# Performance work log

Hardware: AMD Instinct MI355X
Metric: run time of the kernel (lower is better)

The kernel has to match this reference:

```python
import jax, jax.numpy as jnp
import numpy as np

N_NODES = 50000
N_EDGES = 800000


def _gcn_conv(x, src, dst, norm, W, b, num_nodes):
    # x: [N, Fin] -> h: [N, Fout]; messages gathered from src, scattered to dst.
    h = x @ W
    msgs = h[src] * norm[:, None]                      # [E+N, Fout]
    out = jax.ops.segment_sum(msgs, dst, num_segments=num_nodes)
    return out + b


def _gcn_norm(edge_index, num_nodes):
    # Add self-loops and compute symmetric normalization D^-1/2 (A+I) D^-1/2.
    loops = jnp.arange(num_nodes, dtype=edge_index.dtype)
    src = jnp.concatenate([edge_index[0], loops])
    dst = jnp.concatenate([edge_index[1], loops])
    ones = jnp.ones(src.shape[0], dtype=jnp.float32)
    deg = jax.ops.segment_sum(ones, dst, num_segments=num_nodes)
    dinv = jnp.where(deg > 0, jax.lax.rsqrt(jnp.maximum(deg, 1.0)), 0.0)
    norm = dinv[src] * dinv[dst]
    return src, dst, norm


def setup_inputs() -> dict:
    key = jax.random.key(0)
    k1, k2, k3, k4 = jax.random.split(key, 4)
    map_x = jax.random.normal(k1, (N_NODES, 128), dtype=jnp.float32)
    edge_index = jax.random.randint(k2, (2, N_EDGES), 0, N_NODES, dtype=jnp.int64)
    W1 = jax.random.normal(k3, (128, 64), dtype=jnp.float32) * (1.0 / np.sqrt(128))
    b1 = jnp.zeros((64,), dtype=jnp.float32)
    W2 = jax.random.normal(k4, (64, 32), dtype=jnp.float32) * (1.0 / np.sqrt(64))
    b2 = jnp.zeros((32,), dtype=jnp.float32)
    return {"map": map_x, "edge_index": edge_index, "W1": W1, "b1": b1, "W2": W2, "b2": b2}


def reference(map, edge_index, W1, b1, W2, b2):
    num_nodes = map.shape[0]
    src, dst, norm = _gcn_norm(edge_index, num_nodes)
    x = jax.nn.relu(_gcn_conv(map, src, dst, norm, W1, b1, num_nodes))
    x = jax.nn.relu(_gcn_conv(x, src, dst, norm, W2, b2, num_nodes))
    return x
```

## Files before the change

### kernel.cpp

```cpp
#include <hip/hip_runtime.h>

#define TPB 256
#define ACHUNK 4096
#define BSHIFT 6
#define BNODES 64
#define CAP 2048
#define GROWS 128

__device__ __forceinline__ float blo(unsigned u) { return __uint_as_float(u << 16); }
__device__ __forceinline__ float bhi(unsigned u) { return __uint_as_float(u & 0xffff0000u); }
__device__ __forceinline__ unsigned pack2(float a, float b) {
    unsigned ua = __float_as_uint(a); ua += 0x7fffu + ((ua >> 16) & 1u);
    unsigned ub = __float_as_uint(b); ub += 0x7fffu + ((ub >> 16) & 1u);
    return (ua >> 16) | (ub & 0xffff0000u);
}
__device__ __forceinline__ void dec8(uint4 v, float* f) {
    f[0] = blo(v.x); f[1] = bhi(v.x); f[2] = blo(v.y); f[3] = bhi(v.y);
    f[4] = blo(v.z); f[5] = bhi(v.z); f[6] = blo(v.w); f[7] = bhi(v.w);
}
__device__ __forceinline__ void dec4(uint2 v, float* f) {
    f[0] = blo(v.x); f[1] = bhi(v.x); f[2] = blo(v.y); f[3] = bhi(v.y);
}


__global__ __launch_bounds__(TPB) void k_fat(
        const int* __restrict__ src, const int* __restrict__ dst, int E,
        int* __restrict__ bcnt, int* __restrict__ tmp, int NB,
        const float* __restrict__ X, const float* __restrict__ W,
        unsigned int* __restrict__ H1b, int N, int G1, int FB) {
    __shared__ float Ws[128 * 64];
    int* lcnt = (int*)Ws;
    int bid = blockIdx.x;
    int t = threadIdx.x;

    if ((bid % 3) == 0) {
        int fidx = bid / 3;
        if (fidx >= FB) return;
        int c0 = fidx * ACHUNK;
        int s_[16], d_[16];
#pragma unroll
        for (int i = 0; i < 16; i++) {
            int e = c0 + i * TPB + t;
            if (e < E) { s_[i] = src[e]; d_[i] = dst[e]; }
            else d_[i] = -1;
        }
        for (int b = t; b < NB; b += TPB) lcnt[b] = 0;
        __syncthreads();
#pragma unroll
        for (int i = 0; i < 16; i++)
            if (d_[i] >= 0) atomicAdd(&lcnt[d_[i] >> BSHIFT], 1);
        __syncthreads();
        for (int b = t; b < NB; b += TPB) {
            int c = lcnt[b];
            lcnt[b] = c ? (b * CAP + atomicAdd(&bcnt[b], c)) : 0;
        }
        __syncthreads();
#pragma unroll
        for (int i = 0; i < 16; i++) {
            if (d_[i] >= 0) {
                int bkt = d_[i] >> BSHIFT;
                int pos = atomicAdd(&lcnt[bkt], 1);
                if (pos < (bkt + 1) * CAP) {
                    tmp[pos] = ((d_[i] & (BNODES - 1)) << 16) | s_[i];
                }
            }
        }
    } else {
        int gb = bid - bid / 3 - 1;
        if (gb >= G1) return;
        int row0 = gb * GROWS;

        const float4* W4 = (const float4*)W;
        float4* Ws4 = (float4*)Ws;
#pragma unroll
        for (int i = 0; i < 8; i++) Ws4[t + i * 256] = W4[t + i * 256];
        __syncthreads();

        int rg = t >> 3;
        int c0 = (t & 7) * 8;
        int r0 = row0 + rg * 4;
        int ri[4];
#pragma unroll
        for (int i = 0; i < 4; i++) ri[i] = (r0 + i < N) ? (r0 + i) : (N - 1);

        float acc[4][8];
#pragma unroll
        for (int i = 0; i < 4; i++)
#pragma unroll
            for (int j = 0; j < 8; j++) acc[i][j] = 0.0f;

        const float4* X4 = (const float4*)X;
        for (int kk = 0; kk < 32; kk++) {
            float4 xv[4];
#pragma unroll
            for (int i = 0; i < 4; i++) xv[i] = X4[(size_t)ri[i] * 32 + kk];
#pragma unroll
            for (int q = 0; q < 4; q++) {
                const float* w = Ws + (4 * kk + q) * 64 + c0;
                float wq[8];
#pragma unroll
                for (int j = 0; j < 8; j++) wq[j] = w[j];
                float xq[4];
                xq[0] = q == 0 ? xv[0].x : q == 1 ? xv[0].y : q == 2 ? xv[0].z : xv[0].w;
                xq[1] = q == 0 ? xv[1].x : q == 1 ? xv[1].y : q == 2 ? xv[1].z : xv[1].w;
                xq[2] = q == 0 ? xv[2].x : q == 1 ? xv[2].y : q == 2 ? xv[2].z : xv[2].w;
                xq[3] = q == 0 ? xv[3].x : q == 1 ? xv[3].y : q == 2 ? xv[3].z : xv[3].w;
#pragma unroll
                for (int i = 0; i < 4; i++)
#pragma unroll
                    for (int j = 0; j < 8; j++)
                        acc[i][j] = fmaf(xq[i], wq[j], acc[i][j]);
            }
        }
#pragma unroll
        for (int i = 0; i < 4; i++) {
            if (r0 + i < N) {
                uint4 p = { pack2(acc[i][0], acc[i][1]), pack2(acc[i][2], acc[i][3]),
                            pack2(acc[i][4], acc[i][5]), pack2(acc[i][6], acc[i][7]) };
                *(uint4*)(H1b + (size_t)(r0 + i) * 32 + (t & 7) * 4) = p;
            }
        }
    }
}


__global__ __launch_bounds__(TPB) void k_binB(
        const int* __restrict__ bcnt, const int* __restrict__ tmp,
        int* __restrict__ rowptr, unsigned short* __restrict__ rowlen,
        float* __restrict__ dinv, unsigned short* __restrict__ edges,
        const unsigned int* __restrict__ H1b, unsigned int* __restrict__ g1b,
        int N) {
    __shared__ int hist[BNODES];
    __shared__ int cur[BNODES];
    __shared__ int sh[BNODES];
    __shared__ float dl[BNODES];
    int b = blockIdx.x;
    int t = threadIdx.x;
    int node0 = b << BSHIFT;
    int nn = N - node0; if (nn > BNODES) nn = BNODES;
    int cnt = bcnt[b]; if (cnt > CAP) cnt = CAP;
    const int tb = b * CAP;

    if (t < BNODES) hist[t] = 0;
    __syncthreads();
    for (int i = t; i < cnt; i += TPB) atomicAdd(&hist[tmp[tb + i] >> 16], 1);
    __syncthreads();
    if (t < BNODES) sh[t] = hist[t];
    __syncthreads();
    for (int o = 1; o < BNODES; o <<= 1) {
        int x = (t >= o && t < BNODES) ? sh[t - o] : 0;
        __syncthreads();
        if (t < BNODES) sh[t] += x;
        __syncthreads();
    }
    if (t < BNODES) {
        int v = hist[t];
        int excl = sh[t] - v;
        cur[t] = excl;
        float dv = rsqrtf((float)(v + 1));
        dl[t] = dv;
        if (t < nn) {
            dinv[node0 + t] = dv;
            rowptr[node0 + t] = tb + excl;
            rowlen[node0 + t] = (unsigned short)v;
        }
    }
    __syncthreads();
    for (int i = t; i < cnt; i += TPB) {
        int p = tmp[tb + i];
        int pos = atomicAdd(&cur[p >> 16], 1);
        edges[tb + pos] = (unsigned short)(p & 0xffff);
    }
    const uint4* H4 = (const uint4*)H1b;
    uint4* G4 = (uint4*)g1b;
    for (int i = t; i < nn * 8; i += TPB) {
        int r = i >> 3, q = i & 7;
        float dv = dl[r];
        float f[8];
        uint4 hv = H4[(size_t)(node0 + r) * 8 + q];
        dec8(hv, f);
        uint4 p = { pack2(f[0] * dv, f[1] * dv), pack2(f[2] * dv, f[3] * dv),
                    pack2(f[4] * dv, f[5] * dv), pack2(f[6] * dv, f[7] * dv) };
        G4[(size_t)(node0 + r) * 8 + q] = p;
    }
}


__global__ __launch_bounds__(TPB) void k_gg(
        const int* __restrict__ rowptr, const unsigned short* __restrict__ rowlen,
        const unsigned short* __restrict__ edges,
        const unsigned int* __restrict__ g1b,
        const float* __restrict__ dinv, const float* __restrict__ b1,
        const float* __restrict__ W2, unsigned int* __restrict__ g2b, int N) {
    __shared__ float W2s[64 * 32];
    __shared__ float rows[32 * 68];
    __shared__ float dl[32];
    __shared__ int nst[32];
    __shared__ int nlen[32];
    int t = threadIdx.x;
    int node0 = blockIdx.x * 32;
    int nn = N - node0; if (nn > 32) nn = 32;
    if (nn <= 0) return;

    {
        const float4* W4 = (const float4*)W2;
        float4* Wd = (float4*)W2s;
        Wd[t] = W4[t]; Wd[t + 256] = W4[t + 256];
    }
    if (t < nn) {
        dl[t] = dinv[node0 + t];
        nst[t] = rowptr[node0 + t];
        nlen[t] = rowlen[node0 + t];
    }
    __syncthreads();

    const uint4* G4 = (const uint4*)g1b;
    int nl = t >> 3;
    int lane = t & 7;
    if (nl < nn) {
        float acc[8], f[8];
        uint4 sv = G4[(size_t)(node0 + nl) * 8 + lane];
        dec8(sv, acc);
        int base = nst[nl], deg = nlen[nl];
        int j = 0;
        for (; j + 7 < deg; j += 8) {
            uint4 r[8];
#pragma unroll
            for (int u = 0; u < 8; u++)
                r[u] = G4[(size_t)edges[base + j + u] * 8 + lane];
#pragma unroll
            for (int u = 0; u < 8; u++) {
                dec8(r[u], f);
#pragma unroll
                for (int k = 0; k < 8; k++) acc[k] += f[k];
            }
        }
        for (; j < deg; j++) {
            uint4 r0 = G4[(size_t)edges[base + j] * 8 + lane];
            dec8(r0, f);
#pragma unroll
            for (int k = 0; k < 8; k++) acc[k] += f[k];
        }
        float w0 = dl[nl];
        const float4* bb4 = (const float4*)(b1 + lane * 8);
        float4 ba = bb4[0], bc = bb4[1];
        float* rr = rows + nl * 68 + lane * 8;
        rr[0] = fmaxf(fmaf(acc[0], w0, ba.x), 0.0f);
        rr[1] = fmaxf(fmaf(acc[1], w0, ba.y), 0.0f);
        rr[2] = fmaxf(fmaf(acc[2], w0, ba.z), 0.0f);
        rr[3] = fmaxf(fmaf(acc[3], w0, ba.w), 0.0f);
        rr[4] = fmaxf(fmaf(acc[4], w0, bc.x), 0.0f);
        rr[5] = fmaxf(fmaf(acc[5], w0, bc.y), 0.0f);
        rr[6] = fmaxf(fmaf(acc[6], w0, bc.z), 0.0f);
        rr[7] = fmaxf(fmaf(acc[7], w0, bc.w), 0.0f);
    }
    __syncthreads();

    int n = t >> 3;
    int c = t & 7;
    if (n < nn) {
        const float* row = rows + n * 68;
        float a0 = 0.0f, a1 = 0.0f, a2 = 0.0f, a3 = 0.0f;
#pragma unroll 8
        for (int k = 0; k < 64; k++) {
            float rv = row[k];
            const float* w = W2s + k * 32 + 4 * c;
            a0 = fmaf(rv, w[0], a0); a1 = fmaf(rv, w[1], a1);
            a2 = fmaf(rv, w[2], a2); a3 = fmaf(rv, w[3], a3);
        }
        float dv = dl[n];
        uint2 p = { pack2(a0 * dv, a1 * dv), pack2(a2 * dv, a3 * dv) };
        ((uint2*)g2b)[(size_t)(node0 + n) * 8 + c] = p;
    }
}


__global__ __launch_bounds__(TPB) void k_g32(
        const int* __restrict__ rowptr, const unsigned short* __restrict__ rowlen,
        const unsigned short* __restrict__ edges,
        const unsigned int* __restrict__ g2b,
        const float* __restrict__ dinv, const float* __restrict__ b2,
        float* __restrict__ out, int N) {
    __shared__ float dl[32];
    __shared__ int nst[32];
    __shared__ int nlen[32];
    int t = threadIdx.x;
    int node0 = blockIdx.x * 32;
    int nn = N - node0; if (nn > 32) nn = 32;
    if (nn <= 0) return;
    if (t < nn) {
        dl[t] = dinv[node0 + t];
        nst[t] = rowptr[node0 + t];
        nlen[t] = rowlen[node0 + t];
    }
    __syncthreads();

    int nl = t >> 3;
    int lane = t & 7;
    if (nl >= nn) return;

    const uint2* G2 = (const uint2*)g2b;
    float acc[4], f[4];
    uint2 sv = G2[(size_t)(node0 + nl) * 8 + lane];
    dec4(sv, acc);
    int base = nst[nl], deg = nlen[nl];
    int j = 0;
    for (; j + 15 < deg; j += 16) {
        uint2 r[16];
#pragma unroll
        for (int u = 0; u < 16; u++)
            r[u] = G2[(size_t)edges[base + j + u] * 8 + lane];
#pragma unroll
        for (int u = 0; u < 16; u++) {
            dec4(r[u], f);
            acc[0] += f[0]; acc[1] += f[1]; acc[2] += f[2]; acc[3] += f[3];
        }
    }
    for (; j < deg; j++) {
        uint2 r0 = G2[(size_t)edges[base + j] * 8 + lane];
        dec4(r0, f);
        acc[0] += f[0]; acc[1] += f[1]; acc[2] += f[2]; acc[3] += f[3];
    }
    float w0 = dl[nl];
    const float4* bb4 = (const float4*)(b2 + lane * 4);
    float4 ba = bb4[0];
    float4 o0 = { fmaxf(fmaf(acc[0], w0, ba.x), 0.0f),
                  fmaxf(fmaf(acc[1], w0, ba.y), 0.0f),
                  fmaxf(fmaf(acc[2], w0, ba.z), 0.0f),
                  fmaxf(fmaf(acc[3], w0, ba.w), 0.0f) };
    *(float4*)(out + (size_t)(node0 + nl) * 32 + lane * 4) = o0;
}

static inline int cdiv(int a, int b) { return (a + b - 1) / b; }
static inline char* alignup(char* p) { return (char*)(((uintptr_t)p + 255) & ~(uintptr_t)255); }

extern "C" void kernel_launch(void* const* d_in, const int* in_sizes, int n_in,
                              void* d_out, int out_size, void* d_ws, size_t ws_size,
                              hipStream_t stream) {
    const float* x  = (const float*)d_in[0];
    const int*   ei = (const int*)d_in[1];
    const float* W1 = (const float*)d_in[2];
    const float* b1 = (const float*)d_in[3];
    const float* W2 = (const float*)d_in[4];
    const float* b2 = (const float*)d_in[5];
    float* out = (float*)d_out;

    int N = in_sizes[0] / 128;
    int E = in_sizes[1] / 2;
    const int* src = ei;
    const int* dst = ei + E;

    int NB = cdiv(N, BNODES);

    char* p = (char*)d_ws;
    float* dinv  = (float*)p;            p = alignup(p + sizeof(float) * N);
    int* rowptr  = (int*)p;              p = alignup(p + sizeof(int) * N);
    unsigned short* rowlen = (unsigned short*)p;  p = alignup(p + sizeof(short) * N);
    int* bcnt    = (int*)p;              p = alignup(p + sizeof(int) * 1024);
    int* tmp     = (int*)p;              p = alignup(p + sizeof(int) * (size_t)NB * CAP);
    unsigned short* edges = (unsigned short*)p;   p = alignup(p + sizeof(short) * (size_t)NB * CAP);
    unsigned int* h1b = (unsigned int*)p; p = alignup(p + sizeof(short) * (size_t)N * 64);
    unsigned int* g1b = (unsigned int*)p; p = alignup(p + sizeof(short) * (size_t)N * 64);
    unsigned int* g2b = (unsigned int*)p; p = alignup(p + sizeof(short) * (size_t)N * 32);

    dim3 blk(TPB);
    int FB = cdiv(E, ACHUNK);
    int G1 = cdiv(N, GROWS);
    int fat = 1;
    while ((fat + 2) / 3 < FB || fat - (fat + 2) / 3 < G1) fat++;

    hipMemsetAsync(bcnt, 0, sizeof(int) * 1024, stream);
    k_fat<<<fat, blk, 0, stream>>>(src, dst, E, bcnt, tmp, NB,
                                   x, W1, h1b, N, G1, FB);
    k_binB<<<NB, blk, 0, stream>>>(bcnt, tmp, rowptr, rowlen, dinv,
                                   edges, h1b, g1b, N);
    k_gg<<<cdiv(N, 32), blk, 0, stream>>>(rowptr, rowlen, edges, g1b,
                                          dinv, b1, W2, g2b, N);
    k_g32<<<cdiv(N, 32), blk, 0, stream>>>(rowptr, rowlen, edges, g2b,
                                           dinv, b2, out, N);
}
```

Baseline: 152.5 us.

## Drop g1 prescale pass, apply source dinv in gather, vectorize edge index loads

```diff
diff --git a/kernel.cpp b/kernel.cpp
--- a/kernel.cpp
+++ b/kernel.cpp
@@ -124,16 +124,13 @@
 }
 
 
-__global__ __launch_bounds__(TPB) void k_binB(
+__global__ __launch_bounds__(TPB) void k_csr(
         const int* __restrict__ bcnt, const int* __restrict__ tmp,
         int* __restrict__ rowptr, unsigned short* __restrict__ rowlen,
-        float* __restrict__ dinv, unsigned short* __restrict__ edges,
-        const unsigned int* __restrict__ H1b, unsigned int* __restrict__ g1b,
-        int N) {
+        float* __restrict__ dinv, unsigned short* __restrict__ edges, int N) {
     __shared__ int hist[BNODES];
     __shared__ int cur[BNODES];
     __shared__ int sh[BNODES];
-    __shared__ float dl[BNODES];
     int b = blockIdx.x;
     int t = threadIdx.x;
     int node0 = b << BSHIFT;
@@ -141,11 +138,19 @@
     int cnt = bcnt[b]; if (cnt > CAP) cnt = CAP;
     const int tb = b * CAP;
 
+    int v[8];
+#pragma unroll
+    for (int i = 0; i < 8; i++) {
+        int idx = t + i * TPB;
+        v[i] = (idx < cnt) ? tmp[tb + idx] : -1;
+    }
     if (t < BNODES) hist[t] = 0;
     __syncthreads();
-    for (int i = t; i < cnt; i += TPB) atomicAdd(&hist[tmp[tb + i] >> 16], 1);
-    __syncthreads();
-    if (t < BNODES) sh[t] = hist[t];
+#pragma unroll
+    for (int i = 0; i < 8; i++)
+        if (v[i] >= 0) atomicAdd(&hist[v[i] >> 16], 1);
+    __syncthreads();
+    if (t < BNODES) sh[t] = (hist[t] + 7) & ~7;
     __syncthreads();
     for (int o = 1; o < BNODES; o <<= 1) {
         int x = (t >= o && t < BNODES) ? sh[t - o] : 0;
@@ -154,34 +159,24 @@
         __syncthreads();
     }
     if (t < BNODES) {
-        int v = hist[t];
-        int excl = sh[t] - v;
+        int len = hist[t];
+        int excl = sh[t] - ((len + 7) & ~7);
         cur[t] = excl;
-        float dv = rsqrtf((float)(v + 1));
-        dl[t] = dv;
+        float dv = rsqrtf((float)(len + 1));
         if (t < nn) {
             dinv[node0 + t] = dv;
             rowptr[node0 + t] = tb + excl;
-            rowlen[node0 + t] = (unsigned short)v;
-        }
-    }
-    __syncthreads();
-    for (int i = t; i < cnt; i += TPB) {
-        int p = tmp[tb + i];
-        int pos = atomicAdd(&cur[p >> 16], 1);
-        edges[tb + pos] = (unsigned short)(p & 0xffff);
-    }
-    const uint4* H4 = (const uint4*)H1b;
-    uint4* G4 = (uint4*)g1b;
-    for (int i = t; i < nn * 8; i += TPB) {
-        int r = i >> 3, q = i & 7;
-        float dv = dl[r];
-        float f[8];
-        uint4 hv = H4[(size_t)(node0 + r) * 8 + q];
-        dec8(hv, f);
-        uint4 p = { pack2(f[0] * dv, f[1] * dv), pack2(f[2] * dv, f[3] * dv),
-                    pack2(f[4] * dv, f[5] * dv), pack2(f[6] * dv, f[7] * dv) };
-        G4[(size_t)(node0 + r) * 8 + q] = p;
+            rowlen[node0 + t] = (unsigned short)len;
+        }
+    }
+    __syncthreads();
+#pragma unroll
+    for (int i = 0; i < 8; i++) {
+        if (v[i] >= 0) {
+            int pos = atomicAdd(&cur[v[i] >> 16], 1);
+            if (pos < CAP)
+                edges[tb + pos] = (unsigned short)(v[i] & 0xffff);
+        }
     }
 }
 
@@ -189,7 +184,7 @@
 __global__ __launch_bounds__(TPB) void k_gg(
         const int* __restrict__ rowptr, const unsigned short* __restrict__ rowlen,
         const unsigned short* __restrict__ edges,
-        const unsigned int* __restrict__ g1b,
+        const unsigned int* __restrict__ h1b,
         const float* __restrict__ dinv, const float* __restrict__ b1,
         const float* __restrict__ W2, unsigned int* __restrict__ g2b, int N) {
     __shared__ float W2s[64 * 32];
@@ -214,34 +209,46 @@
     }
     __syncthreads();
 
-    const uint4* G4 = (const uint4*)g1b;
+    const uint4* G4 = (const uint4*)h1b;
     int nl = t >> 3;
     int lane = t & 7;
     if (nl < nn) {
         float acc[8], f[8];
+        float w0 = dl[nl];
         uint4 sv = G4[(size_t)(node0 + nl) * 8 + lane];
-        dec8(sv, acc);
+        dec8(sv, f);
+#pragma unroll
+        for (int k = 0; k < 8; k++) acc[k] = w0 * f[k];
         int base = nst[nl], deg = nlen[nl];
         int j = 0;
         for (; j + 7 < deg; j += 8) {
-            uint4 r[8];
-#pragma unroll
-            for (int u = 0; u < 8; u++)
-                r[u] = G4[(size_t)edges[base + j + u] * 8 + lane];
+            uint4 ev = *(const uint4*)(edges + base + j);
+            int s[8];
+            s[0] = ev.x & 0xffff; s[1] = ev.x >> 16;
+            s[2] = ev.y & 0xffff; s[3] = ev.y >> 16;
+            s[4] = ev.z & 0xffff; s[5] = ev.z >> 16;
+            s[6] = ev.w & 0xffff; s[7] = ev.w >> 16;
+            uint4 r[8]; float dv[8];
+#pragma unroll
+            for (int u = 0; u < 8; u++) {
+                r[u] = G4[(size_t)s[u] * 8 + lane];
+                dv[u] = dinv[s[u]];
+            }
 #pragma unroll
             for (int u = 0; u < 8; u++) {
                 dec8(r[u], f);
 #pragma unroll
-                for (int k = 0; k < 8; k++) acc[k] += f[k];
+                for (int k = 0; k < 8; k++) acc[k] = fmaf(dv[u], f[k], acc[k]);
             }
         }
         for (; j < deg; j++) {
-            uint4 r0 = G4[(size_t)edges[base + j] * 8 + lane];
+            int s0 = edges[base + j];
+            float dvx = dinv[s0];
+            uint4 r0 = G4[(size_t)s0 * 8 + lane];
             dec8(r0, f);
 #pragma unroll
-            for (int k = 0; k < 8; k++) acc[k] += f[k];
-        }
-        float w0 = dl[nl];
+            for (int k = 0; k < 8; k++) acc[k] = fmaf(dvx, f[k], acc[k]);
+        }
         const float4* bb4 = (const float4*)(b1 + lane * 8);
         float4 ba = bb4[0], bc = bb4[1];
         float* rr = rows + nl * 68 + lane * 8;
@@ -306,12 +313,32 @@
     int base = nst[nl], deg = nlen[nl];
     int j = 0;
     for (; j + 15 < deg; j += 16) {
+        uint4 ea = *(const uint4*)(edges + base + j);
+        uint4 eb = *(const uint4*)(edges + base + j + 8);
+        int s[16];
+        s[0]  = ea.x & 0xffff; s[1]  = ea.x >> 16; s[2]  = ea.y & 0xffff; s[3]  = ea.y >> 16;
+        s[4]  = ea.z & 0xffff; s[5]  = ea.z >> 16; s[6]  = ea.w & 0xffff; s[7]  = ea.w >> 16;
+        s[8]  = eb.x & 0xffff; s[9]  = eb.x >> 16; s[10] = eb.y & 0xffff; s[11] = eb.y >> 16;
+        s[12] = eb.z & 0xffff; s[13] = eb.z >> 16; s[14] = eb.w & 0xffff; s[15] = eb.w >> 16;
         uint2 r[16];
 #pragma unroll
-        for (int u = 0; u < 16; u++)
-            r[u] = G2[(size_t)edges[base + j + u] * 8 + lane];
+        for (int u = 0; u < 16; u++) r[u] = G2[(size_t)s[u] * 8 + lane];
 #pragma unroll
         for (int u = 0; u < 16; u++) {
+            dec4(r[u], f);
+            acc[0] += f[0]; acc[1] += f[1]; acc[2] += f[2]; acc[3] += f[3];
+        }
+    }
+    for (; j + 7 < deg; j += 8) {
+        uint4 ea = *(const uint4*)(edges + base + j);
+        int s[8];
+        s[0] = ea.x & 0xffff; s[1] = ea.x >> 16; s[2] = ea.y & 0xffff; s[3] = ea.y >> 16;
+        s[4] = ea.z & 0xffff; s[5] = ea.z >> 16; s[6] = ea.w & 0xffff; s[7] = ea.w >> 16;
+        uint2 r[8];
+#pragma unroll
+        for (int u = 0; u < 8; u++) r[u] = G2[(size_t)s[u] * 8 + lane];
+#pragma unroll
+        for (int u = 0; u < 8; u++) {
             dec4(r[u], f);
             acc[0] += f[0]; acc[1] += f[1]; acc[2] += f[2]; acc[3] += f[3];
         }
@@ -360,7 +387,6 @@
     int* tmp     = (int*)p;              p = alignup(p + sizeof(int) * (size_t)NB * CAP);
     unsigned short* edges = (unsigned short*)p;   p = alignup(p + sizeof(short) * (size_t)NB * CAP);
     unsigned int* h1b = (unsigned int*)p; p = alignup(p + sizeof(short) * (size_t)N * 64);
-    unsigned int* g1b = (unsigned int*)p; p = alignup(p + sizeof(short) * (size_t)N * 64);
     unsigned int* g2b = (unsigned int*)p; p = alignup(p + sizeof(short) * (size_t)N * 32);
 
     dim3 blk(TPB);
@@ -372,9 +398,8 @@
     hipMemsetAsync(bcnt, 0, sizeof(int) * 1024, stream);
     k_fat<<<fat, blk, 0, stream>>>(src, dst, E, bcnt, tmp, NB,
                                    x, W1, h1b, N, G1, FB);
-    k_binB<<<NB, blk, 0, stream>>>(bcnt, tmp, rowptr, rowlen, dinv,
-                                   edges, h1b, g1b, N);
-    k_gg<<<cdiv(N, 32), blk, 0, stream>>>(rowptr, rowlen, edges, g1b,
+    k_csr<<<NB, blk, 0, stream>>>(bcnt, tmp, rowptr, rowlen, dinv, edges, N);
+    k_gg<<<cdiv(N, 32), blk, 0, stream>>>(rowptr, rowlen, edges, h1b,
                                           dinv, b1, W2, g2b, N);
     k_g32<<<cdiv(N, 32), blk, 0, stream>>>(rowptr, rowlen, edges, g2b,
                                            dinv, b2, out, N);
```

New measurement: 149.1 us. -2.2%, faster.
